# Optimization experiments

Hardware: AMD Instinct MI355X
Metric: run time of the kernel (lower is better)

The kernel has to match this reference:

```python
import jax, jax.numpy as jnp
import numpy as np


def gcn_conv(x, src, dst, W, b, num_nodes):
    # PyG GCNConv with add_self_loops=True, symmetric normalization.
    # src/dst already include self-loops.
    ones = jnp.ones(src.shape[0], dtype=x.dtype)
    deg = jax.ops.segment_sum(ones, dst, num_segments=num_nodes)  # [N]
    dinv = jnp.where(deg > 0, jax.lax.rsqrt(deg), 0.0)
    norm = dinv[src] * dinv[dst]                                   # [E+N]
    h = x @ W                                                      # [N, out]
    msg = h[src] * norm[:, None]                                   # gather + scale
    out = jax.ops.segment_sum(msg, dst, num_segments=num_nodes)    # scatter-add
    return out + b


def setup_inputs() -> dict:
    key = jax.random.key(0)
    k1, k2, k3, k4 = jax.random.split(key, 4)
    N, E = 50000, 1600000
    IN, HID, OUT = 1536, 256, 128
    x = jax.random.normal(k1, (N, IN), dtype=jnp.float32)
    edge_index = jax.random.randint(k2, (2, E), 0, N, dtype=jnp.int64)
    # Glorot-style scaled weights
    W1 = jax.random.normal(k3, (IN, HID), dtype=jnp.float32) / np.sqrt(IN)
    W2 = jax.random.normal(k4, (HID, OUT), dtype=jnp.float32) / np.sqrt(HID)
    b1 = jnp.zeros((HID,), dtype=jnp.float32)
    b2 = jnp.zeros((OUT,), dtype=jnp.float32)
    return {"x": x, "edge_index": edge_index, "W1": W1, "b1": b1,
            "W2": W2, "b2": b2, "num_nodes": N}


def reference(x, edge_index, W1, b1, W2, b2, num_nodes):
    loop = jnp.arange(num_nodes, dtype=edge_index.dtype)
    src = jnp.concatenate([edge_index[0], loop])
    dst = jnp.concatenate([edge_index[1], loop])
    h = gcn_conv(x, src, dst, W1, b1, num_nodes)
    h = jax.nn.relu(h)
    h = gcn_conv(h, src, dst, W2, b2, num_nodes)
    # F.normalize(h, dim=1): x / max(||x||_2, 1e-12)
    nrm = jnp.linalg.norm(h, axis=1, keepdims=True)
    return h / jnp.maximum(nrm, 1e-12)
```

## Files before the change

### kernel.cpp

```cpp
#include <hip/hip_runtime.h>

typedef __attribute__((ext_vector_type(4))) float f32x4;
typedef __attribute__((ext_vector_type(2))) float f32x2;
typedef __attribute__((ext_vector_type(8))) short s16x8;

static __device__ __forceinline__ unsigned short f2bf(float f) {
  unsigned int u = __builtin_bit_cast(unsigned int, f);
  u += 0x7fffu + ((u >> 16) & 1u);
  return (unsigned short)(u >> 16);
}
static __device__ __forceinline__ float bf2f(unsigned short h) {
  unsigned int u = ((unsigned int)h) << 16;
  return __builtin_bit_cast(float, u);
}

static __device__ __forceinline__ void gload_lds16(const void* g, void* l) {
  __builtin_amdgcn_global_load_lds(
      (const __attribute__((address_space(1))) unsigned int*)g,
      (__attribute__((address_space(3))) unsigned int*)l, 16, 0, 0);
}

__global__ void zero_k(int* p, int n) {
  int i = blockIdx.x * 256 + threadIdx.x;
  if (i < n) p[i] = 0;
}
__global__ void deg_count_k(const int* __restrict__ edges, int* cnt, int E) {
  int e = blockIdx.x * 256 + threadIdx.x;
  if (e < E) atomicAdd(&cnt[edges[E + e]], 1);
}

__global__ __launch_bounds__(256) void scan1_k(const int* __restrict__ cnt,
                                               int* __restrict__ loc,
                                               int* __restrict__ bsum, int N) {
  int t = threadIdx.x;
  int i0 = blockIdx.x * 1024 + t * 4;
  int c[4];
#pragma unroll
  for (int j = 0; j < 4; ++j) c[j] = (i0 + j < N) ? cnt[i0 + j] : 0;
  int tsum = c[0] + c[1] + c[2] + c[3];
  int lane = t & 63, wv = t >> 6;
  int incl = tsum;
#pragma unroll
  for (int off = 1; off < 64; off <<= 1) {
    int u = __shfl_up(incl, off, 64);
    if (lane >= off) incl += u;
  }
  __shared__ int ws[4];
  if (lane == 63) ws[wv] = incl;
  __syncthreads();
  int wbase = 0;
  for (int w = 0; w < wv; ++w) wbase += ws[w];
  int run = wbase + incl - tsum;
#pragma unroll
  for (int j = 0; j < 4; ++j) {
    if (i0 + j < N) loc[i0 + j] = run;
    run += c[j];
  }
  if (t == 255) bsum[blockIdx.x] = wbase + incl;
}
__global__ void scan2_k(int* bsum, int nb) {
  int lane = threadIdx.x;
  int v = (lane < nb) ? bsum[lane] : 0;
  int incl = v;
#pragma unroll
  for (int off = 1; off < 64; off <<= 1) {
    int u = __shfl_up(incl, off, 64);
    if (lane >= off) incl += u;
  }
  if (lane < nb) bsum[lane] = incl - v;
}
__global__ void addoff_k(int* loc, int* cursor, const int* __restrict__ bsum,
                         const int* __restrict__ cnt, float* __restrict__ dinv, int N) {
  int i = blockIdx.x * 256 + threadIdx.x;
  if (i < N) {
    int v = loc[i] + bsum[i >> 10];
    loc[i] = v;
    cursor[i] = v;
    dinv[i] = rsqrtf((float)(cnt[i] + 1));
  }
}
__global__ void fill_k(const int* __restrict__ edges, int* cursor,
                       int* __restrict__ csr, int E) {
  int e = blockIdx.x * 256 + threadIdx.x;
  if (e < E) {
    int s = edges[e], d = edges[E + e];
    int pos = atomicAdd(&cursor[d], 1);
    csr[pos] = s;
  }
}

__global__ __launch_bounds__(256) void convw_k(const float* __restrict__ W,
                                               unsigned short* __restrict__ Wt,
                                               int K, int Nn) {
  __shared__ float t[32][33];
  const int tx = threadIdx.x & 31, ty = threadIdx.x >> 5;
  const int k0 = blockIdx.x * 32, n0 = blockIdx.y * 32;
#pragma unroll
  for (int r = 0; r < 32; r += 8)
    t[r + ty][tx] = W[(long long)(k0 + r + ty) * Nn + (n0 + tx)];
  __syncthreads();
#pragma unroll
  for (int r = 0; r < 32; r += 8)
    Wt[(long long)(n0 + r + ty) * K + (k0 + tx)] = f2bf(t[tx][r + ty]);
}

template <int KTOT, int NTOT, bool A_BF16>
__global__ __launch_bounds__(256, 2) void gemm_k(
    const void* __restrict__ Aptr, const unsigned short* __restrict__ Bt,
    const float* __restrict__ dinv, unsigned short* __restrict__ outg, int M) {
  constexpr int BM = 128, BK = 32;
  constexpr int LDA = BK + 8;
  constexpr int MI = BM / 16;
  constexpr int STRIP = NTOT / 4;
  constexpr int NF = STRIP / 16;
  constexpr int BCH = (NTOT / 16) / 4;
  constexpr int ACH = (BM / 16) / 4;
  constexpr int NT = KTOT / BK;
  constexpr int TPR = 256 / BM;
  constexpr int FPT = BK / TPR;
  constexpr int ASZ = A_BF16 ? (BM * BK) : (BM * LDA);
  constexpr int VM_N = A_BF16 ? 4 : 12;

  __shared__ unsigned short Asm_[3][ASZ];
  __shared__ unsigned short Bsm_[3][NTOT * BK];

  const int tid = threadIdx.x;
  const int wave = tid >> 6;
  const int lane = tid & 63;
  const int fr = lane & 15;
  const int quad = lane >> 4;
  const int m0 = blockIdx.x * BM;

  f32x4 acc[MI][NF];
#pragma unroll
  for (int i = 0; i < MI; ++i)
#pragma unroll
    for (int j = 0; j < NF; ++j) { f32x4 z = {0.f, 0.f, 0.f, 0.f}; acc[i][j] = z; }

  const int sl_r = lane >> 2;
  const int sl_s = (lane & 3) ^ ((lane >> 3) & 3);

  auto stageB = [&](int k0, int buf) {
#pragma unroll
    for (int c = 0; c < BCH; ++c) {
      int cc = wave * BCH + c;
      int r = cc * 16 + sl_r;
      const unsigned short* gp = Bt + (long long)r * KTOT + k0 + sl_s * 8;
      gload_lds16(gp, &Bsm_[buf][cc * 512]);
    }
  };
  auto stageA_h = [&](int k0, int buf) {
    const unsigned short* Ah = (const unsigned short*)Aptr;
#pragma unroll
    for (int c = 0; c < ACH; ++c) {
      int cc = wave * ACH + c;
      int r = cc * 16 + sl_r;
      const unsigned short* gp = Ah + (long long)(m0 + r) * KTOT + k0 + sl_s * 8;
      gload_lds16(gp, &Asm_[buf][cc * 512]);
    }
  };

  const int sr = tid / TPR;
  const int sc = (tid % TPR) * FPT;
  const int arow = min(m0 + sr, M - 1);
  const float* arowf = (const float*)Aptr + (long long)arow * KTOT;
  float va0[FPT], va1[FPT], va2[FPT];

#define LOADA(VA, K0)                                                          \
  do {                                                                         \
    _Pragma("unroll") for (int c = 0; c < FPT / 4; ++c) {                      \
      f32x4 v = __builtin_nontemporal_load(                                    \
          (const f32x4*)(arowf + (K0) + sc + c * 4));                          \
      _Pragma("unroll") for (int j = 0; j < 4; ++j) VA[c * 4 + j] = v[j];      \
    }                                                                          \
  } while (0)

#define CVTWA(VA, BUF)                                                         \
  do {                                                                         \
    _Pragma("unroll") for (int c = 0; c < FPT / 8; ++c) {                      \
      s16x8 hh;                                                                \
      _Pragma("unroll") for (int j = 0; j < 8; ++j)                            \
          hh[j] = (short)f2bf(VA[c * 8 + j]);                                  \
      *(s16x8*)&Asm_[BUF][sr * LDA + sc + c * 8] = hh;                         \
    }                                                                          \
  } while (0)

  const int xsl = (fr >> 1) & 3;
  auto compute = [&](int cur) {
    s16x8 af[MI], bfr[NF];
#pragma unroll
    for (int mi = 0; mi < MI; ++mi) {
      if constexpr (A_BF16)
        af[mi] = *(const s16x8*)&Asm_[cur][(mi * 16 + fr) * BK + ((quad ^ xsl) << 3)];
      else
        af[mi] = *(const s16x8*)&Asm_[cur][(mi * 16 + fr) * LDA + quad * 8];
    }
#pragma unroll
    for (int ni = 0; ni < NF; ++ni)
      bfr[ni] = *(const s16x8*)&Bsm_[cur][(wave * STRIP + ni * 16 + fr) * BK + ((quad ^ xsl) << 3)];
#pragma unroll
    for (int mi = 0; mi < MI; ++mi)
#pragma unroll
      for (int ni = 0; ni < NF; ++ni)
        acc[mi][ni] = __builtin_amdgcn_mfma_f32_16x16x32_bf16(af[mi], bfr[ni], acc[mi][ni], 0, 0, 0);
  };

  if constexpr (A_BF16) {
    stageB(0, 0); stageA_h(0, 0);
    stageB(BK, 1); stageA_h(BK, 1);
  } else {
    {
      float vt[FPT];
      LOADA(vt, 0);  CVTWA(vt, 0);
      LOADA(vt, BK); CVTWA(vt, 1);
    }
    stageB(0, 0);
    stageB(BK, 1);
    __builtin_amdgcn_sched_barrier(0);
    LOADA(va0, 2 * BK);
    LOADA(va1, 3 * BK);
    LOADA(va2, 4 * BK);
  }

#define GITER(J, P, PS, VA)                                                    \
  {                                                                            \
    if constexpr (VM_N == 12)                                                  \
      asm volatile("s_waitcnt vmcnt(12) lgkmcnt(0)" ::: "memory");             \
    else                                                                       \
      asm volatile("s_waitcnt vmcnt(4) lgkmcnt(0)" ::: "memory");              \
    __builtin_amdgcn_s_barrier();                                              \
    __builtin_amdgcn_sched_barrier(0);                                         \
    int ks_ = ((J) + 2 < NT) ? ((J) + 2) * BK : (KTOT - BK);                   \
    stageB(ks_, (PS));                                                         \
    if constexpr (A_BF16) {                                                    \
      stageA_h(ks_, (PS));                                                     \
    } else {                                                                   \
      __builtin_amdgcn_sched_barrier(0);   \
      CVTWA(VA, (PS));                                                         \
      int kl_ = ((J) + 5 < NT) ? ((J) + 5) * BK : (KTOT - BK);                 \
      LOADA(VA, kl_);                                                          \
    }                                                                          \
    compute(P);                                                                \
  }

  int j = 0;
  for (; j + 3 <= NT; j += 3) {
    GITER(j, 0, 2, va0);
    GITER(j + 1, 1, 0, va1);
    GITER(j + 2, 2, 1, va2);
  }
  if constexpr (NT % 3 >= 1) GITER(j, 0, 2, va0);
  if constexpr (NT % 3 == 2) GITER(j + 1, 1, 0, va1);

#undef GITER
#undef LOADA
#undef CVTWA

#pragma unroll
  for (int mi = 0; mi < MI; ++mi) {
    int mbase = mi * 16 + quad * 4;
#pragma unroll
    for (int r = 0; r < 4; ++r) {
      int gm = m0 + mbase + r;
      if (gm < M) {
        float dv = dinv[gm];
#pragma unroll
        for (int ni = 0; ni < NF; ++ni) {
          int col = wave * STRIP + ni * 16 + fr;
          outg[(long long)gm * NTOT + col] = f2bf(acc[mi][ni][r] * dv);
        }
      }
    }
  }
}

__global__ __launch_bounds__(256) void agg1_k(const int* __restrict__ csr,
                                              const int* __restrict__ row,
                                              const int* __restrict__ cnt,
                                              const unsigned short* __restrict__ g,
                                              const float* __restrict__ bias,
                                              const float* __restrict__ dinv,
                                              unsigned short* __restrict__ h, int N) {
  const int wave = threadIdx.x >> 6, lane = threadIdx.x & 63;
  const int node = blockIdx.x * 4 + wave;
  if (node >= N) return;
  const int grp = lane >> 5, sub = lane & 31;
  const int f0 = sub * 8;
  float s[8];
#pragma unroll
  for (int k = 0; k < 8; ++k) s[k] = 0.0f;
  const int start = row[node], len = cnt[node];
  int j = 0;
  for (; j + 8 <= len; j += 8) {
    int idx[4];
#pragma unroll
    for (int t = 0; t < 4; ++t) idx[t] = csr[start + j + t * 2 + grp];
    s16x8 v[4];
#pragma unroll
    for (int t = 0; t < 4; ++t) v[t] = *(const s16x8*)&g[(long long)idx[t] * 256 + f0];
#pragma unroll
    for (int t = 0; t < 4; ++t)
#pragma unroll
      for (int k = 0; k < 8; ++k) s[k] += bf2f((unsigned short)v[t][k]);
  }
  for (; j < len; j += 2) {
    int jt = j + grp;
    bool val = jt < len;
    int idx = csr[start + (val ? jt : 0)];
    s16x8 v = *(const s16x8*)&g[(long long)idx * 256 + f0];
    float m = val ? 1.0f : 0.0f;
#pragma unroll
    for (int k = 0; k < 8; ++k) s[k] += m * bf2f((unsigned short)v[k]);
  }
#pragma unroll
  for (int k = 0; k < 8; ++k) s[k] += __shfl_xor(s[k], 32, 64);
  s16x8 sv = *(const s16x8*)&g[(long long)node * 256 + f0];
#pragma unroll
  for (int k = 0; k < 8; ++k) s[k] += bf2f((unsigned short)sv[k]);
  const float dv = dinv[node];
  f32x4 b0 = *(const f32x4*)&bias[f0];
  f32x4 b1v = *(const f32x4*)&bias[f0 + 4];
  if (grp == 0) {
    s16x8 o;
#pragma unroll
    for (int k = 0; k < 4; ++k) o[k] = (short)f2bf(fmaxf(0.0f, b0[k] + dv * s[k]));
#pragma unroll
    for (int k = 0; k < 4; ++k) o[4 + k] = (short)f2bf(fmaxf(0.0f, b1v[k] + dv * s[4 + k]));
    *(s16x8*)&h[(long long)node * 256 + f0] = o;
  }
}

__global__ __launch_bounds__(256) void agg2_k(const int* __restrict__ csr,
                                              const int* __restrict__ row,
                                              const int* __restrict__ cnt,
                                              const unsigned short* __restrict__ g,
                                              const float* __restrict__ b2,
                                              const float* __restrict__ dinv,
                                              float* __restrict__ out, int N) {
  const int wave = threadIdx.x >> 6, lane = threadIdx.x & 63;
  const int node = blockIdx.x * 4 + wave;
  if (node >= N) return;
  const int grp = lane >> 4, sub = lane & 15;
  const int f0 = sub * 8;
  float s[8];
#pragma unroll
  for (int k = 0; k < 8; ++k) s[k] = 0.0f;
  const int start = row[node], len = cnt[node];
  int j = 0;
  for (; j + 8 <= len; j += 8) {
    int idx[2];
#pragma unroll
    for (int t = 0; t < 2; ++t) idx[t] = csr[start + j + t * 4 + grp];
    s16x8 v[2];
#pragma unroll
    for (int t = 0; t < 2; ++t) v[t] = *(const s16x8*)&g[(long long)idx[t] * 128 + f0];
#pragma unroll
    for (int t = 0; t < 2; ++t)
#pragma unroll
      for (int k = 0; k < 8; ++k) s[k] += bf2f((unsigned short)v[t][k]);
  }
  for (; j < len; j += 4) {
    int jt = j + grp;
    bool val = jt < len;
    int idx = csr[start + (val ? jt : 0)];
    s16x8 v = *(const s16x8*)&g[(long long)idx * 128 + f0];
    float m = val ? 1.0f : 0.0f;
#pragma unroll
    for (int k = 0; k < 8; ++k) s[k] += m * bf2f((unsigned short)v[k]);
  }
#pragma unroll
  for (int k = 0; k < 8; ++k) s[k] += __shfl_xor(s[k], 16, 64);
#pragma unroll
  for (int k = 0; k < 8; ++k) s[k] += __shfl_xor(s[k], 32, 64);
  s16x8 sv = *(const s16x8*)&g[(long long)node * 128 + f0];
#pragma unroll
  for (int k = 0; k < 8; ++k) s[k] += bf2f((unsigned short)sv[k]);
  const float dv = dinv[node];
  f32x4 b0 = *(const f32x4*)&b2[f0];
  f32x4 b1v = *(const f32x4*)&b2[f0 + 4];
  float x[8];
#pragma unroll
  for (int k = 0; k < 4; ++k) x[k] = b0[k] + dv * s[k];
#pragma unroll
  for (int k = 0; k < 4; ++k) x[4 + k] = b1v[k] + dv * s[4 + k];
  float ss = 0.0f;
#pragma unroll
  for (int k = 0; k < 8; ++k) ss += x[k] * x[k];
#pragma unroll
  for (int off = 1; off < 16; off <<= 1) ss += __shfl_xor(ss, off, 64);
  const float inv = 1.0f / fmaxf(sqrtf(ss), 1e-12f);
  if (grp == 0) {
    f32x4 o0 = {x[0] * inv, x[1] * inv, x[2] * inv, x[3] * inv};
    f32x4 o1 = {x[4] * inv, x[5] * inv, x[6] * inv, x[7] * inv};
    *(f32x4*)&out[(long long)node * 128 + f0] = o0;
    *(f32x4*)&out[(long long)node * 128 + f0 + 4] = o1;
  }
}

extern "C" void kernel_launch(void* const* d_in, const int* in_sizes, int n_in,
                              void* d_out, int out_size, void* d_ws, size_t ws_size,
                              hipStream_t stream) {
  const float* x = (const float*)d_in[0];
  const int* edges = (const int*)d_in[1];
  const float* W1 = (const float*)d_in[2];
  const float* b1 = (const float*)d_in[3];
  const float* W2 = (const float*)d_in[4];
  const float* b2 = (const float*)d_in[5];
  float* out = (float*)d_out;

  const int HID = in_sizes[3];
  const int OUT = in_sizes[5];
  const int IN = in_sizes[2] / HID;
  const int N = in_sizes[0] / IN;
  const int E = in_sizes[1] / 2;

  size_t off = 0;
  auto carve = [&](size_t bytes) {
    void* p = (char*)d_ws + off;
    off += (bytes + 255) & ~(size_t)255;
    return p;
  };
  int* cnt = (int*)carve((size_t)N * 4);
  int* cursor = (int*)carve((size_t)N * 4);
  int* row = (int*)carve((size_t)N * 4);
  int* bsum = (int*)carve(64 * 4);
  int* csr = (int*)carve((size_t)E * 4 + 1024);
  float* dinv = (float*)carve((size_t)N * 4);
  unsigned short* W1t = (unsigned short*)carve((size_t)IN * HID * 2);
  unsigned short* W2t = (unsigned short*)carve((size_t)HID * OUT * 2);
  unsigned short* g1 = (unsigned short*)carve((size_t)N * HID * 2);
  unsigned short* acc1 = (unsigned short*)carve((size_t)N * HID * 2);
  unsigned short* g2 = (unsigned short*)carve((size_t)N * OUT * 2);
  (void)ws_size; (void)n_in; (void)out_size;

  const int nb = (N + 1023) / 1024;

  zero_k<<<(N + 255) / 256, 256, 0, stream>>>(cnt, N);
  deg_count_k<<<(E + 255) / 256, 256, 0, stream>>>(edges, cnt, E);

  scan1_k<<<nb, 256, 0, stream>>>(cnt, row, bsum, N);
  scan2_k<<<1, 64, 0, stream>>>(bsum, nb);
  addoff_k<<<(N + 255) / 256, 256, 0, stream>>>(row, cursor, bsum, cnt, dinv, N);
  fill_k<<<(E + 255) / 256, 256, 0, stream>>>(edges, cursor, csr, E);

  convw_k<<<dim3(IN / 32, HID / 32), 256, 0, stream>>>(W1, W1t, IN, HID);
  convw_k<<<dim3(HID / 32, OUT / 32), 256, 0, stream>>>(W2, W2t, HID, OUT);

  int mtiles = (N + 127) / 128;
  gemm_k<1536, 256, false><<<mtiles, 256, 0, stream>>>(x, W1t, dinv, g1, N);
  agg1_k<<<(N + 3) / 4, 256, 0, stream>>>(csr, row, cnt, g1, b1, dinv, acc1, N);
  gemm_k<256, 128, true><<<mtiles, 256, 0, stream>>>(acc1, W2t, dinv, g2, N);
  agg2_k<<<(N + 3) / 4, 256, 0, stream>>>(csr, row, cnt, g2, b2, dinv, out, N);
}
```

Baseline: 891.8 us.

## Fuse layer-2 GEMM into layer-1 aggregation and simplify gather layouts

Folds the second GEMM (h @ W2, scaled by dinv) into the layer-1 aggregation kernel. Each block converts W2 into a bf16 LDS copy, and each wave computes its node's 128 outputs from an LDS row buffer, which removes the acc1 intermediate round trip, the W2 transpose kernel and the second GEMM launch. The aggregation kernels now use one wave per node, with each lane gathering 4 or 2 contiguous features and 8 outstanding neighbor loads, instead of splitting edges across lane groups. The catch is a persistent 512-block grid that re-converts W2 in every block, and a scalar FMA matvec on CUDA cores in place of MFMA.

```diff
diff --git a/kernel.cpp b/kernel.cpp
--- a/kernel.cpp
+++ b/kernel.cpp
@@ -3,6 +3,8 @@
 typedef __attribute__((ext_vector_type(4))) float f32x4;
 typedef __attribute__((ext_vector_type(2))) float f32x2;
 typedef __attribute__((ext_vector_type(8))) short s16x8;
+typedef __attribute__((ext_vector_type(4))) unsigned short u16x4;
+typedef __attribute__((ext_vector_type(2))) unsigned short u16x2;
 
 static __device__ __forceinline__ unsigned short f2bf(float f) {
   unsigned int u = __builtin_bit_cast(unsigned int, f);
@@ -104,8 +106,8 @@
     Wt[(long long)(n0 + r + ty) * K + (k0 + tx)] = f2bf(t[tx][r + ty]);
 }
 
-template <int KTOT, int NTOT, bool A_BF16>
-__global__ __launch_bounds__(256, 2) void gemm_k(
+template <int KTOT, int NTOT>
+__global__ __launch_bounds__(256, 2) void gemm1_k(
     const void* __restrict__ Aptr, const unsigned short* __restrict__ Bt,
     const float* __restrict__ dinv, unsigned short* __restrict__ outg, int M) {
   constexpr int BM = 128, BK = 32;
@@ -114,14 +116,11 @@
   constexpr int STRIP = NTOT / 4;
   constexpr int NF = STRIP / 16;
   constexpr int BCH = (NTOT / 16) / 4;
-  constexpr int ACH = (BM / 16) / 4;
   constexpr int NT = KTOT / BK;
   constexpr int TPR = 256 / BM;
   constexpr int FPT = BK / TPR;
-  constexpr int ASZ = A_BF16 ? (BM * BK) : (BM * LDA);
-  constexpr int VM_N = A_BF16 ? 4 : 12;
-
-  __shared__ unsigned short Asm_[3][ASZ];
+
+  __shared__ unsigned short Asm_[3][BM * LDA];
   __shared__ unsigned short Bsm_[3][NTOT * BK];
 
   const int tid = threadIdx.x;
@@ -147,16 +146,6 @@
       int r = cc * 16 + sl_r;
       const unsigned short* gp = Bt + (long long)r * KTOT + k0 + sl_s * 8;
       gload_lds16(gp, &Bsm_[buf][cc * 512]);
-    }
-  };
-  auto stageA_h = [&](int k0, int buf) {
-    const unsigned short* Ah = (const unsigned short*)Aptr;
-#pragma unroll
-    for (int c = 0; c < ACH; ++c) {
-      int cc = wave * ACH + c;
-      int r = cc * 16 + sl_r;
-      const unsigned short* gp = Ah + (long long)(m0 + r) * KTOT + k0 + sl_s * 8;
-      gload_lds16(gp, &Asm_[buf][cc * 512]);
     }
   };
 
@@ -189,12 +178,8 @@
   auto compute = [&](int cur) {
     s16x8 af[MI], bfr[NF];
 #pragma unroll
-    for (int mi = 0; mi < MI; ++mi) {
-      if constexpr (A_BF16)
-        af[mi] = *(const s16x8*)&Asm_[cur][(mi * 16 + fr) * BK + ((quad ^ xsl) << 3)];
-      else
-        af[mi] = *(const s16x8*)&Asm_[cur][(mi * 16 + fr) * LDA + quad * 8];
-    }
+    for (int mi = 0; mi < MI; ++mi)
+      af[mi] = *(const s16x8*)&Asm_[cur][(mi * 16 + fr) * LDA + quad * 8];
 #pragma unroll
     for (int ni = 0; ni < NF; ++ni)
       bfr[ni] = *(const s16x8*)&Bsm_[cur][(wave * STRIP + ni * 16 + fr) * BK + ((quad ^ xsl) << 3)];
@@ -205,41 +190,29 @@
         acc[mi][ni] = __builtin_amdgcn_mfma_f32_16x16x32_bf16(af[mi], bfr[ni], acc[mi][ni], 0, 0, 0);
   };
 
-  if constexpr (A_BF16) {
-    stageB(0, 0); stageA_h(0, 0);
-    stageB(BK, 1); stageA_h(BK, 1);
-  } else {
-    {
-      float vt[FPT];
-      LOADA(vt, 0);  CVTWA(vt, 0);
-      LOADA(vt, BK); CVTWA(vt, 1);
-    }
-    stageB(0, 0);
-    stageB(BK, 1);
-    __builtin_amdgcn_sched_barrier(0);
-    LOADA(va0, 2 * BK);
-    LOADA(va1, 3 * BK);
-    LOADA(va2, 4 * BK);
-  }
+  {
+    float vt[FPT];
+    LOADA(vt, 0);  CVTWA(vt, 0);
+    LOADA(vt, BK); CVTWA(vt, 1);
+  }
+  stageB(0, 0);
+  stageB(BK, 1);
+  __builtin_amdgcn_sched_barrier(0);
+  LOADA(va0, 2 * BK);
+  LOADA(va1, 3 * BK);
+  LOADA(va2, 4 * BK);
 
 #define GITER(J, P, PS, VA)                                                    \
   {                                                                            \
-    if constexpr (VM_N == 12)                                                  \
-      asm volatile("s_waitcnt vmcnt(12) lgkmcnt(0)" ::: "memory");             \
-    else                                                                       \
-      asm volatile("s_waitcnt vmcnt(4) lgkmcnt(0)" ::: "memory");              \
+    asm volatile("s_waitcnt vmcnt(12) lgkmcnt(0)" ::: "memory");               \
     __builtin_amdgcn_s_barrier();                                              \
     __builtin_amdgcn_sched_barrier(0);                                         \
     int ks_ = ((J) + 2 < NT) ? ((J) + 2) * BK : (KTOT - BK);                   \
     stageB(ks_, (PS));                                                         \
-    if constexpr (A_BF16) {                                                    \
-      stageA_h(ks_, (PS));                                                     \
-    } else {                                                                   \
-      __builtin_amdgcn_sched_barrier(0);   \
-      CVTWA(VA, (PS));                                                         \
-      int kl_ = ((J) + 5 < NT) ? ((J) + 5) * BK : (KTOT - BK);                 \
-      LOADA(VA, kl_);                                                          \
-    }                                                                          \
+    __builtin_amdgcn_sched_barrier(0);                                         \
+    CVTWA(VA, (PS));                                                           \
+    int kl_ = ((J) + 5 < NT) ? ((J) + 5) * BK : (KTOT - BK);                   \
+    LOADA(VA, kl_);                                                            \
     compute(P);                                                                \
   }
 
@@ -274,59 +247,72 @@
   }
 }
 
-__global__ __launch_bounds__(256) void agg1_k(const int* __restrict__ csr,
-                                              const int* __restrict__ row,
-                                              const int* __restrict__ cnt,
-                                              const unsigned short* __restrict__ g,
-                                              const float* __restrict__ bias,
-                                              const float* __restrict__ dinv,
-                                              unsigned short* __restrict__ h, int N) {
+__global__ __launch_bounds__(512) void agg1f_k(const int* __restrict__ csr,
+                                               const int* __restrict__ row,
+                                               const int* __restrict__ cnt,
+                                               const unsigned short* __restrict__ g,
+                                               const float* __restrict__ b1,
+                                               const float* __restrict__ W2,
+                                               const float* __restrict__ dinv,
+                                               unsigned short* __restrict__ g2,
+                                               int N) {
+  __shared__ unsigned short W2s[256 * 128];
+  __shared__ float rowb[8][260];
+
+  for (int i = threadIdx.x; i < 256 * 128; i += 512)
+    W2s[i] = f2bf(W2[i]);
+  __syncthreads();
+
   const int wave = threadIdx.x >> 6, lane = threadIdx.x & 63;
-  const int node = blockIdx.x * 4 + wave;
-  if (node >= N) return;
-  const int grp = lane >> 5, sub = lane & 31;
-  const int f0 = sub * 8;
-  float s[8];
-#pragma unroll
-  for (int k = 0; k < 8; ++k) s[k] = 0.0f;
-  const int start = row[node], len = cnt[node];
-  int j = 0;
-  for (; j + 8 <= len; j += 8) {
-    int idx[4];
-#pragma unroll
-    for (int t = 0; t < 4; ++t) idx[t] = csr[start + j + t * 2 + grp];
-    s16x8 v[4];
-#pragma unroll
-    for (int t = 0; t < 4; ++t) v[t] = *(const s16x8*)&g[(long long)idx[t] * 256 + f0];
-#pragma unroll
-    for (int t = 0; t < 4; ++t)
-#pragma unroll
-      for (int k = 0; k < 8; ++k) s[k] += bf2f((unsigned short)v[t][k]);
-  }
-  for (; j < len; j += 2) {
-    int jt = j + grp;
-    bool val = jt < len;
-    int idx = csr[start + (val ? jt : 0)];
-    s16x8 v = *(const s16x8*)&g[(long long)idx * 256 + f0];
-    float m = val ? 1.0f : 0.0f;
-#pragma unroll
-    for (int k = 0; k < 8; ++k) s[k] += m * bf2f((unsigned short)v[k]);
-  }
-#pragma unroll
-  for (int k = 0; k < 8; ++k) s[k] += __shfl_xor(s[k], 32, 64);
-  s16x8 sv = *(const s16x8*)&g[(long long)node * 256 + f0];
-#pragma unroll
-  for (int k = 0; k < 8; ++k) s[k] += bf2f((unsigned short)sv[k]);
-  const float dv = dinv[node];
-  f32x4 b0 = *(const f32x4*)&bias[f0];
-  f32x4 b1v = *(const f32x4*)&bias[f0 + 4];
-  if (grp == 0) {
-    s16x8 o;
-#pragma unroll
-    for (int k = 0; k < 4; ++k) o[k] = (short)f2bf(fmaxf(0.0f, b0[k] + dv * s[k]));
-#pragma unroll
-    for (int k = 0; k < 4; ++k) o[4 + k] = (short)f2bf(fmaxf(0.0f, b1v[k] + dv * s[4 + k]));
-    *(s16x8*)&h[(long long)node * 256 + f0] = o;
+  const int f0 = lane << 2;
+  float* myrow = &rowb[wave][0];
+
+  for (int node = blockIdx.x * 8 + wave; node < N; node += gridDim.x * 8) {
+    u16x4 sv = *(const u16x4*)&g[(long long)node * 256 + f0];
+    f32x4 s = {bf2f(sv[0]), bf2f(sv[1]), bf2f(sv[2]), bf2f(sv[3])};
+    const int start = row[node], len = cnt[node];
+    int j = 0;
+    for (; j + 8 <= len; j += 8) {
+      int idx[8];
+#pragma unroll
+      for (int t = 0; t < 8; ++t) idx[t] = csr[start + j + t];
+      u16x4 v[8];
+#pragma unroll
+      for (int t = 0; t < 8; ++t) v[t] = *(const u16x4*)&g[(long long)idx[t] * 256 + f0];
+#pragma unroll
+      for (int t = 0; t < 8; ++t) {
+        s[0] += bf2f(v[t][0]); s[1] += bf2f(v[t][1]);
+        s[2] += bf2f(v[t][2]); s[3] += bf2f(v[t][3]);
+      }
+    }
+    for (; j < len; ++j) {
+      int i0 = csr[start + j];
+      u16x4 v = *(const u16x4*)&g[(long long)i0 * 256 + f0];
+      s[0] += bf2f(v[0]); s[1] += bf2f(v[1]); s[2] += bf2f(v[2]); s[3] += bf2f(v[3]);
+    }
+    const float dv = dinv[node];
+    f32x4 b = *(const f32x4*)&b1[f0];
+    f32x4 h;
+#pragma unroll
+    for (int k = 0; k < 4; ++k) h[k] = fmaxf(0.0f, b[k] + dv * s[k]);
+
+    *(f32x4*)&myrow[f0] = h;
+    float ga = 0.0f, gb = 0.0f;
+    float ga2 = 0.0f, gb2 = 0.0f;
+#pragma unroll 4
+    for (int kk = 0; kk < 64; ++kk) {
+      f32x4 hv = *(const f32x4*)&myrow[kk * 4];
+#pragma unroll
+      for (int t = 0; t < 4; ++t) {
+        unsigned int wp = *(const unsigned int*)&W2s[(kk * 4 + t) * 128 + lane * 2];
+        float w0 = bf2f((unsigned short)(wp & 0xffffu));
+        float w1 = bf2f((unsigned short)(wp >> 16));
+        if (t & 1) { ga2 += hv[t] * w0; gb2 += hv[t] * w1; }
+        else       { ga  += hv[t] * w0; gb  += hv[t] * w1; }
+      }
+    }
+    u16x2 o = {f2bf(dv * (ga + ga2)), f2bf(dv * (gb + gb2))};
+    *(u16x2*)&g2[(long long)node * 128 + lane * 2] = o;
   }
 }
 
@@ -337,64 +323,39 @@
                                               const float* __restrict__ b2,
                                               const float* __restrict__ dinv,
                                               float* __restrict__ out, int N) {
-  const int wave = threadIdx.x >> 6, lane = threadIdx.x & 63;
-  const int node = blockIdx.x * 4 + wave;
+  int node = blockIdx.x * 4 + (threadIdx.x >> 6);
   if (node >= N) return;
-  const int grp = lane >> 4, sub = lane & 15;
-  const int f0 = sub * 8;
-  float s[8];
-#pragma unroll
-  for (int k = 0; k < 8; ++k) s[k] = 0.0f;
-  const int start = row[node], len = cnt[node];
+  int lane = threadIdx.x & 63;
+  int f0 = lane << 1;
+  u16x2 sv = *(const u16x2*)&g[(long long)node * 128 + f0];
+  float s0 = bf2f(sv[0]), s1 = bf2f(sv[1]);
+  int start = row[node], len = cnt[node];
   int j = 0;
   for (; j + 8 <= len; j += 8) {
-    int idx[2];
-#pragma unroll
-    for (int t = 0; t < 2; ++t) idx[t] = csr[start + j + t * 4 + grp];
-    s16x8 v[2];
-#pragma unroll
-    for (int t = 0; t < 2; ++t) v[t] = *(const s16x8*)&g[(long long)idx[t] * 128 + f0];
-#pragma unroll
-    for (int t = 0; t < 2; ++t)
-#pragma unroll
-      for (int k = 0; k < 8; ++k) s[k] += bf2f((unsigned short)v[t][k]);
-  }
-  for (; j < len; j += 4) {
-    int jt = j + grp;
-    bool val = jt < len;
-    int idx = csr[start + (val ? jt : 0)];
-    s16x8 v = *(const s16x8*)&g[(long long)idx * 128 + f0];
-    float m = val ? 1.0f : 0.0f;
-#pragma unroll
-    for (int k = 0; k < 8; ++k) s[k] += m * bf2f((unsigned short)v[k]);
-  }
-#pragma unroll
-  for (int k = 0; k < 8; ++k) s[k] += __shfl_xor(s[k], 16, 64);
-#pragma unroll
-  for (int k = 0; k < 8; ++k) s[k] += __shfl_xor(s[k], 32, 64);
-  s16x8 sv = *(const s16x8*)&g[(long long)node * 128 + f0];
-#pragma unroll
-  for (int k = 0; k < 8; ++k) s[k] += bf2f((unsigned short)sv[k]);
-  const float dv = dinv[node];
-  f32x4 b0 = *(const f32x4*)&b2[f0];
-  f32x4 b1v = *(const f32x4*)&b2[f0 + 4];
-  float x[8];
-#pragma unroll
-  for (int k = 0; k < 4; ++k) x[k] = b0[k] + dv * s[k];
-#pragma unroll
-  for (int k = 0; k < 4; ++k) x[4 + k] = b1v[k] + dv * s[4 + k];
-  float ss = 0.0f;
-#pragma unroll
-  for (int k = 0; k < 8; ++k) ss += x[k] * x[k];
-#pragma unroll
-  for (int off = 1; off < 16; off <<= 1) ss += __shfl_xor(ss, off, 64);
-  const float inv = 1.0f / fmaxf(sqrtf(ss), 1e-12f);
-  if (grp == 0) {
-    f32x4 o0 = {x[0] * inv, x[1] * inv, x[2] * inv, x[3] * inv};
-    f32x4 o1 = {x[4] * inv, x[5] * inv, x[6] * inv, x[7] * inv};
-    *(f32x4*)&out[(long long)node * 128 + f0] = o0;
-    *(f32x4*)&out[(long long)node * 128 + f0 + 4] = o1;
-  }
+    int idx[8];
+#pragma unroll
+    for (int t = 0; t < 8; ++t) idx[t] = csr[start + j + t];
+    u16x2 v[8];
+#pragma unroll
+    for (int t = 0; t < 8; ++t) v[t] = *(const u16x2*)&g[(long long)idx[t] * 128 + f0];
+#pragma unroll
+    for (int t = 0; t < 8; ++t) { s0 += bf2f(v[t][0]); s1 += bf2f(v[t][1]); }
+  }
+  for (; j < len; ++j) {
+    int i0 = csr[start + j];
+    u16x2 v = *(const u16x2*)&g[(long long)i0 * 128 + f0];
+    s0 += bf2f(v[0]); s1 += bf2f(v[1]);
+  }
+  float dv = dinv[node];
+  f32x2 b = *(const f32x2*)&b2[f0];
+  float x0 = b[0] + dv * s0;
+  float x1 = b[1] + dv * s1;
+  float ss = x0 * x0 + x1 * x1;
+#pragma unroll
+  for (int off = 32; off > 0; off >>= 1) ss += __shfl_xor(ss, off, 64);
+  float inv = 1.0f / fmaxf(sqrtf(ss), 1e-12f);
+  f32x2 o = {x0 * inv, x1 * inv};
+  *(f32x2*)&out[(long long)node * 128 + f0] = o;
 }
 
 extern "C" void kernel_launch(void* const* d_in, const int* in_sizes, int n_in,
@@ -413,6 +374,7 @@
   const int IN = in_sizes[2] / HID;
   const int N = in_sizes[0] / IN;
   const int E = in_sizes[1] / 2;
+  (void)OUT;
 
   size_t off = 0;
   auto carve = [&](size_t bytes) {
@@ -427,9 +389,7 @@
   int* csr = (int*)carve((size_t)E * 4 + 1024);
   float* dinv = (float*)carve((size_t)N * 4);
   unsigned short* W1t = (unsigned short*)carve((size_t)IN * HID * 2);
-  unsigned short* W2t = (unsigned short*)carve((size_t)HID * OUT * 2);
   unsigned short* g1 = (unsigned short*)carve((size_t)N * HID * 2);
-  unsigned short* acc1 = (unsigned short*)carve((size_t)N * HID * 2);
   unsigned short* g2 = (unsigned short*)carve((size_t)N * OUT * 2);
   (void)ws_size; (void)n_in; (void)out_size;
 
@@ -444,11 +404,9 @@
   fill_k<<<(E + 255) / 256, 256, 0, stream>>>(edges, cursor, csr, E);
 
   convw_k<<<dim3(IN / 32, HID / 32), 256, 0, stream>>>(W1, W1t, IN, HID);
-  convw_k<<<dim3(HID / 32, OUT / 32), 256, 0, stream>>>(W2, W2t, HID, OUT);
 
   int mtiles = (N + 127) / 128;
-  gemm_k<1536, 256, false><<<mtiles, 256, 0, stream>>>(x, W1t, dinv, g1, N);
-  agg1_k<<<(N + 3) / 4, 256, 0, stream>>>(csr, row, cnt, g1, b1, dinv, acc1, N);
-  gemm_k<256, 128, true><<<mtiles, 256, 0, stream>>>(acc1, W2t, dinv, g2, N);
+  gemm1_k<1536, 256><<<mtiles, 256, 0, stream>>>(x, W1t, dinv, g1, N);
+  agg1f_k<<<512, 512, 0, stream>>>(csr, row, cnt, g1, b1, W2, dinv, g2, N);
   agg2_k<<<(N + 3) / 4, 256, 0, stream>>>(csr, row, cnt, g2, b2, dinv, out, N);
 }
```

New measurement: 940.1 us. 5.4% more time.
